# Kernel tuning notes

Measured on AMD Instinct MI355X. Metric: run time of the kernel, lower is better.

Reference implementation:

```python
import jax, jax.numpy as jnp
import numpy as np

N_HEADS = 8
MAX_PARTS = 8
TOKENS_PER_PART = 64
NUM_BLOCKS = 6
D_MODEL = 256
LN_EPS = 1e-5


def layernorm(x, w, b):
    mu = jnp.mean(x, axis=-1, keepdims=True)
    var = jnp.var(x, axis=-1, keepdims=True)
    return (x - mu) * jax.lax.rsqrt(var + LN_EPS) * w + b


def mha(q, k, v, in_w, in_b, out_w, out_b):
    # torch nn.MultiheadAttention: packed in_proj [3D, D], out_proj [D, D]
    D = q.shape[-1]
    dh = D // N_HEADS
    wq, wk, wv = in_w[:D], in_w[D:2 * D], in_w[2 * D:]
    bq, bk, bv = in_b[:D], in_b[D:2 * D], in_b[2 * D:]
    qp = q @ wq.T + bq  # [B, Sq, D]
    kp = k @ wk.T + bk
    vp = v @ wv.T + bv
    B, Sq, _ = qp.shape
    Sk = kp.shape[1]
    qh = qp.reshape(B, Sq, N_HEADS, dh).transpose(0, 2, 1, 3)
    kh = kp.reshape(B, Sk, N_HEADS, dh).transpose(0, 2, 1, 3)
    vh = vp.reshape(B, Sk, N_HEADS, dh).transpose(0, 2, 1, 3)
    scores = jnp.einsum('bhqd,bhkd->bhqk', qh, kh) / jnp.sqrt(jnp.asarray(dh, qp.dtype))
    attn = jax.nn.softmax(scores, axis=-1)
    out = jnp.einsum('bhqk,bhkd->bhqd', attn, vh)
    out = out.transpose(0, 2, 1, 3).reshape(B, Sq, D)
    return out @ out_w.T + out_b


def setup_inputs() -> dict:
    key = jax.random.key(0)
    ks = jax.random.split(key, 16)
    s = 0.02
    return {
        'feat': jax.random.normal(ks[0], (64, 49, 512), jnp.float32),
        'img_proj_w': jax.random.normal(ks[1], (256, 512), jnp.float32) * s,
        'img_proj_b': jnp.zeros((256,), jnp.float32),
        'init_part_tokens': jax.random.normal(ks[2], (512, 256), jnp.float32),
        'part_id_emb': jax.random.normal(ks[3], (8, 256), jnp.float32),
        'local_in_w': jax.random.normal(ks[4], (768, 256), jnp.float32) * s,
        'local_in_b': jnp.zeros((768,), jnp.float32),
        'local_out_w': jax.random.normal(ks[5], (256, 256), jnp.float32) * s,
        'local_out_b': jnp.zeros((256,), jnp.float32),
        'cross_in_w': jax.random.normal(ks[6], (768, 256), jnp.float32) * s,
        'cross_in_b': jnp.zeros((768,), jnp.float32),
        'cross_out_w': jax.random.normal(ks[7], (256, 256), jnp.float32) * s,
        'cross_out_b': jnp.zeros((256,), jnp.float32),
        'norm1_w': jnp.ones((6, 256), jnp.float32),
        'norm1_b': jnp.zeros((6, 256), jnp.float32),
        'norm2_w': jnp.ones((6, 256), jnp.float32),
        'norm2_b': jnp.zeros((6, 256), jnp.float32),
        'coord_w': jax.random.normal(ks[8], (3, 256), jnp.float32) * s,
        'coord_b': jnp.zeros((3,), jnp.float32),
    }


def reference(feat, img_proj_w, img_proj_b, init_part_tokens, part_id_emb,
              local_in_w, local_in_b, local_out_w, local_out_b,
              cross_in_w, cross_in_b, cross_out_w, cross_out_b,
              norm1_w, norm1_b, norm2_w, norm2_b, coord_w, coord_b):
    B = feat.shape[0]
    P, T, D = MAX_PARTS, TOKENS_PER_PART, D_MODEL
    img_tokens = feat @ img_proj_w.T + img_proj_b  # [B, 49, D]
    # broadcast part-id embedding over tokens_per_part
    pid = jnp.repeat(part_id_emb, T, axis=0)  # [P*T, D]
    st = jnp.broadcast_to(init_part_tokens + pid, (B, P * T, D))
    for i in range(NUM_BLOCKS):
        # block-diagonal local attention: fold parts into batch dim
        parts = st.reshape(B * P, T, D)
        local = mha(parts, parts, parts, local_in_w, local_in_b, local_out_w, local_out_b)
        local = local.reshape(B, P * T, D)
        st = layernorm(st + local, norm1_w[i], norm1_b[i])
        cross = mha(st, img_tokens, img_tokens, cross_in_w, cross_in_b, cross_out_w, cross_out_b)
        st = layernorm(st + cross, norm2_w[i], norm2_b[i])
    coords = st @ coord_w.T + coord_b
    return coords.reshape(B, P, T, 3)
```

## Files before the change

kernel.cpp:

```cpp
#include <hip/hip_runtime.h>
#include <hip/hip_bf16.h>


#define B_     64
#define P_     8
#define T_     64
#define S_     512
#define D_     256
#define H_     8
#define DH_    32
#define NIMG_  49
#define M_ST   32768
#define M_IMG  3136

#define AS1 __attribute__((address_space(1)))
#define AS3 __attribute__((address_space(3)))

typedef short bf16x8 __attribute__((ext_vector_type(8)));
typedef float f32x4  __attribute__((ext_vector_type(4)));

__device__ inline uint f2b_pk(float x, float y) {
    uint bx = __float_as_uint(x), by = __float_as_uint(y);
    bx = (bx + 0x7FFFu + ((bx >> 16) & 1u)) >> 16;
    by = (by + 0x7FFFu + ((by >> 16) & 1u)) >> 16;
    return bx | (by << 16);
}
__device__ inline ushort f2b(float x) {
    uint b = __float_as_uint(x);
    return (ushort)((b + 0x7FFFu + ((b >> 16) & 1u)) >> 16);
}
__device__ inline float b2f(ushort u) {
    return __uint_as_float(((uint)u) << 16);
}

__global__ __launch_bounds__(256) void cvt_bf16x4(
    const float4* __restrict__ in, uint2* __restrict__ out, int n4)
{
    int i = blockIdx.x * 256 + threadIdx.x;
    if (i < n4) {
        float4 v = in[i];
        out[i] = make_uint2(f2b_pk(v.x, v.y), f2b_pk(v.z, v.w));
    }
}

__global__ __launch_bounds__(256) void gemm_bf16(
    const ushort* __restrict__ A,
    const ushort* __restrict__ W,
    const float*  __restrict__ bias,
    ushort*       __restrict__ C,
    int M, int N, int K)
{
    __shared__ ushort smem[128 * 128];
    ushort* Asm = smem;
    ushort* Bsm = smem + 4096;

    const int tid  = threadIdx.x;
    const int lane = tid & 63;
    const int wave = tid >> 6;
    const int wr = wave >> 1, wc = wave & 1;
    const int row0 = blockIdx.x * 128, col0 = blockIdx.y * 128;

    f32x4 acc[4][4] = {};

    const int skc = (tid & 3) * 8;
    const int sr0 = tid >> 2;
    const int fr  = lane & 15;
    const int g   = lane >> 4;

    for (int k0 = 0; k0 < K; k0 += 32) {
        #pragma unroll
        for (int i = 0; i < 2; ++i) {
            const int r = sr0 + i * 64;
            const int e = (tid + i * 256) * 8;
            int ra = row0 + r; if (ra >= M) ra = M - 1;
            __builtin_amdgcn_global_load_lds(
                (const AS1 void*)(A + (size_t)ra * K + k0 + skc),
                (AS3 void*)&Asm[e], 16, 0, 0);
            __builtin_amdgcn_global_load_lds(
                (const AS1 void*)(W + (size_t)(col0 + r) * K + k0 + skc),
                (AS3 void*)&Bsm[e], 16, 0, 0);
        }
        __syncthreads();

        bf16x8 af[4], bf[4];
        #pragma unroll
        for (int i = 0; i < 4; ++i)
            af[i] = *reinterpret_cast<const bf16x8*>(&Asm[(wr * 64 + i * 16 + fr) * 32 + g * 8]);
        #pragma unroll
        for (int j = 0; j < 4; ++j)
            bf[j] = *reinterpret_cast<const bf16x8*>(&Bsm[(wc * 64 + j * 16 + fr) * 32 + g * 8]);
        #pragma unroll
        for (int i = 0; i < 4; ++i)
            #pragma unroll
            for (int j = 0; j < 4; ++j)
                acc[i][j] = __builtin_amdgcn_mfma_f32_16x16x32_bf16(
                    af[i], bf[j], acc[i][j], 0, 0, 0);
        __syncthreads();
    }

    float bn[4];
    #pragma unroll
    for (int j = 0; j < 4; ++j) bn[j] = bias[col0 + wc * 64 + j * 16 + fr];

    #pragma unroll
    for (int i = 0; i < 4; ++i)
        #pragma unroll
        for (int j = 0; j < 4; ++j)
            #pragma unroll
            for (int r = 0; r < 4; ++r)
                smem[(wr * 64 + i * 16 + g * 4 + r) * 128 + wc * 64 + j * 16 + fr] =
                    f2b(acc[i][j][r] + bn[j]);
    __syncthreads();

    #pragma unroll
    for (int it = 0; it < 8; ++it) {
        const int elem = (it * 256 + tid) * 8;
        const int lrow = elem >> 7, lcol = elem & 127;
        const int m = row0 + lrow;
        if (m < M)
            *reinterpret_cast<uint4*>(&C[(size_t)m * N + col0 + lcol]) =
                *reinterpret_cast<const uint4*>(&smem[elem]);
    }
}

__global__ __launch_bounds__(512, 4) void gemm_bf16_big(
    const ushort* __restrict__ A,
    const ushort* __restrict__ W,
    const float*  __restrict__ bias,
    ushort*       __restrict__ C,
    int N, int K)
{
    __shared__ ushort smem[16384];
    ushort* Asm = smem;
    ushort* Bsm = smem + 8192;

    const int tid  = threadIdx.x;
    const int lane = tid & 63;
    const int wave = tid >> 6;
    const int wr = wave >> 1, wc = wave & 1;
    const int row0 = blockIdx.x * 256, col0 = blockIdx.y * 128;

    f32x4 acc[4][4] = {};
    const int skc = (tid & 3) * 8;
    const int sr0 = tid >> 2;
    const int fr  = lane & 15;
    const int g   = lane >> 4;

    for (int k0 = 0; k0 < K; k0 += 32) {
        #pragma unroll
        for (int i = 0; i < 2; ++i) {
            const int r = sr0 + i * 128;
            __builtin_amdgcn_global_load_lds(
                (const AS1 void*)(A + (size_t)(row0 + r) * K + k0 + skc),
                (AS3 void*)&Asm[(tid + i * 512) * 8], 16, 0, 0);
        }
        __builtin_amdgcn_global_load_lds(
            (const AS1 void*)(W + (size_t)(col0 + sr0) * K + k0 + skc),
            (AS3 void*)&Bsm[tid * 8], 16, 0, 0);
        __syncthreads();

        bf16x8 af[4], bf[4];
        #pragma unroll
        for (int i = 0; i < 4; ++i)
            af[i] = *reinterpret_cast<const bf16x8*>(&Asm[(wr * 64 + i * 16 + fr) * 32 + g * 8]);
        #pragma unroll
        for (int j = 0; j < 4; ++j)
            bf[j] = *reinterpret_cast<const bf16x8*>(&Bsm[(wc * 64 + j * 16 + fr) * 32 + g * 8]);
        #pragma unroll
        for (int i = 0; i < 4; ++i)
            #pragma unroll
            for (int j = 0; j < 4; ++j)
                acc[i][j] = __builtin_amdgcn_mfma_f32_16x16x32_bf16(
                    af[i], bf[j], acc[i][j], 0, 0, 0);
        __syncthreads();
    }

    float bn[4];
    #pragma unroll
    for (int j = 0; j < 4; ++j) bn[j] = bias[col0 + wc * 64 + j * 16 + fr];

    #pragma unroll
    for (int h2 = 0; h2 < 2; ++h2) {
        if ((wr >> 1) == h2) {
            const int lwr = wr & 1;
            #pragma unroll
            for (int i = 0; i < 4; ++i)
                #pragma unroll
                for (int j = 0; j < 4; ++j)
                    #pragma unroll
                    for (int r = 0; r < 4; ++r)
                        smem[(lwr * 64 + i * 16 + g * 4 + r) * 128 + wc * 64 + j * 16 + fr] =
                            f2b(acc[i][j][r] + bn[j]);
        }
        __syncthreads();
        #pragma unroll
        for (int it = 0; it < 4; ++it) {
            const int elem = (it * 512 + tid) * 8;
            const int lrow = elem >> 7, lcol = elem & 127;
            *reinterpret_cast<uint4*>(
                &C[(size_t)(row0 + h2 * 128 + lrow) * N + col0 + lcol]) =
                *reinterpret_cast<const uint4*>(&smem[elem]);
        }
        __syncthreads();
    }
}

__global__ __launch_bounds__(256) void gemm_ln(
    const ushort* __restrict__ A,
    const ushort* __restrict__ W,
    const float*  __restrict__ bias,
    ushort*       __restrict__ stb,
    const float*  __restrict__ lnw,
    const float*  __restrict__ lnb)
{
    __shared__ ushort As[64 * 32];
    __shared__ ushort Bs[256 * 32];
    __shared__ ushort Cs[64 * 256];
    __shared__ float  redS[64][4];
    __shared__ float  redS2[64][4];

    const int tid  = threadIdx.x;
    const int lane = tid & 63;
    const int wc   = tid >> 6;
    const int fr = lane & 15, g = lane >> 4;
    const int row0 = blockIdx.x * 64;

    f32x4 acc[4][4] = {};
    const int skc = (tid & 3) * 8;
    const int sr  = tid >> 2;

    for (int k0 = 0; k0 < 256; k0 += 32) {
        __builtin_amdgcn_global_load_lds(
            (const AS1 void*)(A + (size_t)(row0 + sr) * 256 + k0 + skc),
            (AS3 void*)&As[tid * 8], 16, 0, 0);
        #pragma unroll
        for (int q = 0; q < 4; ++q)
            __builtin_amdgcn_global_load_lds(
                (const AS1 void*)(W + (size_t)(sr + q * 64) * 256 + k0 + skc),
                (AS3 void*)&Bs[(tid + q * 256) * 8], 16, 0, 0);
        __syncthreads();

        bf16x8 af[4], bf[4];
        #pragma unroll
        for (int i = 0; i < 4; ++i)
            af[i] = *reinterpret_cast<const bf16x8*>(&As[(i * 16 + fr) * 32 + g * 8]);
        #pragma unroll
        for (int j = 0; j < 4; ++j)
            bf[j] = *reinterpret_cast<const bf16x8*>(&Bs[(wc * 64 + j * 16 + fr) * 32 + g * 8]);
        #pragma unroll
        for (int i = 0; i < 4; ++i)
            #pragma unroll
            for (int j = 0; j < 4; ++j)
                acc[i][j] = __builtin_amdgcn_mfma_f32_16x16x32_bf16(
                    af[i], bf[j], acc[i][j], 0, 0, 0);
        __syncthreads();
    }

    int   col[4]; float bv[4], wv[4], lb[4];
    #pragma unroll
    for (int j = 0; j < 4; ++j) {
        col[j] = wc * 64 + j * 16 + fr;
        bv[j]  = bias[col[j]];
        wv[j]  = lnw[col[j]];
        lb[j]  = lnb[col[j]];
    }

    #pragma unroll
    for (int i = 0; i < 4; ++i)
        #pragma unroll
        for (int r = 0; r < 4; ++r) {
            const int rl = i * 16 + g * 4 + r;
            const size_t rb = (size_t)(row0 + rl) * 256;
            float s = 0.f, s2 = 0.f;
            #pragma unroll
            for (int j = 0; j < 4; ++j) {
                float x = acc[i][j][r] + bv[j] + b2f(stb[rb + col[j]]);
                acc[i][j][r] = x;
                s += x; s2 += x * x;
            }
            #pragma unroll
            for (int o = 1; o < 16; o <<= 1) {
                s  += __shfl_xor(s, o);
                s2 += __shfl_xor(s2, o);
            }
            if (fr == 0) { redS[rl][wc] = s; redS2[rl][wc] = s2; }
        }
    __syncthreads();

    #pragma unroll
    for (int i = 0; i < 4; ++i)
        #pragma unroll
        for (int r = 0; r < 4; ++r) {
            const int rl = i * 16 + g * 4 + r;
            const float ts  = redS[rl][0] + redS[rl][1] + redS[rl][2] + redS[rl][3];
            const float ts2 = redS2[rl][0] + redS2[rl][1] + redS2[rl][2] + redS2[rl][3];
            const float mean = ts * (1.f / 256.f);
            const float var  = ts2 * (1.f / 256.f) - mean * mean;
            const float rs   = rsqrtf(var + 1e-5f);
            #pragma unroll
            for (int j = 0; j < 4; ++j) {
                const float y = (acc[i][j][r] - mean) * rs * wv[j] + lb[j];
                Cs[rl * 256 + col[j]] = f2b(y);
            }
        }
    __syncthreads();

    #pragma unroll
    for (int it = 0; it < 8; ++it) {
        const int elem = (it * 256 + tid) * 8;
        const int rl = elem >> 8, c = elem & 255;
        *reinterpret_cast<uint4*>(&stb[(size_t)(row0 + rl) * 256 + c]) =
            *reinterpret_cast<const uint4*>(&Cs[elem]);
    }
}

template<int CROSS>
__global__ __launch_bounds__(256) void attn_mfma(
    const ushort* __restrict__ qsrc,
    const ushort* __restrict__ ksrc,
    const ushort* __restrict__ vsrc,
    ushort* __restrict__ out)
{
    constexpr int QSTR = CROSS ? 256 : 768;
    constexpr int KSTR = CROSS ? 256 : 768;

    const int bid = blockIdx.x;
    int qrow0, krow0;
    if (CROSS) { qrow0 = (bid >> 3) * 512 + (bid & 7) * 64; krow0 = (bid >> 3) * 49; }
    else       { qrow0 = bid * 64; krow0 = bid * 64; }

    __shared__ ushort P_lds[4][64][72];
    __shared__ ushort Vt_lds[4][32][72];
    ushort* Os = &P_lds[0][0][0];

    const int tid = threadIdx.x;
    const int w = tid >> 6, l = tid & 63;
    const int fr = l & 15, g = l >> 4;
    ushort (*P)[72]  = P_lds[w];
    ushort (*Vt)[72] = Vt_lds[w];

    f32x4 o2[2][4][2] = {};

    #pragma unroll
    for (int hh = 0; hh < 2; ++hh) {
        const int h = w + hh * 4;
        const int hoff = h * 32;

        bf16x8 kf[4], qf[4];
        #pragma unroll
        for (int i = 0; i < 4; ++i) {
            int t = 16 * i + fr;
            if (CROSS && t > 48) t = 48;
            kf[i] = *reinterpret_cast<const bf16x8*>(
                ksrc + (size_t)(krow0 + t) * KSTR + hoff + g * 8);
        }
        #pragma unroll
        for (int j = 0; j < 4; ++j)
            qf[j] = *reinterpret_cast<const bf16x8*>(
                qsrc + (size_t)(qrow0 + 16 * j + fr) * QSTR + hoff + g * 8);

        #pragma unroll
        for (int t2 = 0; t2 < 2; ++t2) {
            const int task = t2 * 64 + l;
            const int rp = task >> 2, cg = task & 3;
            int r0 = 2 * rp, r1 = r0 + 1;
            if (CROSS) { if (r0 > 48) r0 = 48; if (r1 > 48) r1 = 48; }
            const uint4 a = *reinterpret_cast<const uint4*>(
                vsrc + (size_t)(krow0 + r0) * KSTR + hoff + cg * 8);
            const uint4 b = *reinterpret_cast<const uint4*>(
                vsrc + (size_t)(krow0 + r1) * KSTR + hoff + cg * 8);
            const uint ac[4] = {a.x, a.y, a.z, a.w};
            const uint bc[4] = {b.x, b.y, b.z, b.w};
            #pragma unroll
            for (int k = 0; k < 4; ++k) {
                uint lo = (ac[k] & 0xFFFFu) | (bc[k] << 16);
                uint hi = (ac[k] >> 16)     | (bc[k] & 0xFFFF0000u);
                *reinterpret_cast<uint*>(&Vt[cg * 8 + 2 * k][2 * rp])     = lo;
                *reinterpret_cast<uint*>(&Vt[cg * 8 + 2 * k + 1][2 * rp]) = hi;
            }
        }

        f32x4 st_[4][4];
        #pragma unroll
        for (int i = 0; i < 4; ++i)
            #pragma unroll
            for (int j = 0; j < 4; ++j) {
                f32x4 z = {};
                st_[i][j] = __builtin_amdgcn_mfma_f32_16x16x32_bf16(
                    kf[i], qf[j], z, 0, 0, 0);
                st_[i][j] *= 0.17677669529663689f;
            }
        if (CROSS) {
            #pragma unroll
            for (int j = 0; j < 4; ++j)
                #pragma unroll
                for (int r = 0; r < 4; ++r)
                    if (r > 0 || g > 0) st_[3][j][r] = -1e30f;
        }

        #pragma unroll
        for (int j = 0; j < 4; ++j) {
            float mx = -1e30f;
            #pragma unroll
            for (int i = 0; i < 4; ++i)
                #pragma unroll
                for (int r = 0; r < 4; ++r) mx = fmaxf(mx, st_[i][j][r]);
            mx = fmaxf(mx, __shfl_xor(mx, 16));
            mx = fmaxf(mx, __shfl_xor(mx, 32));
            float sm = 0.f;
            #pragma unroll
            for (int i = 0; i < 4; ++i)
                #pragma unroll
                for (int r = 0; r < 4; ++r) {
                    float p = __expf(st_[i][j][r] - mx);
                    st_[i][j][r] = p;
                    sm += p;
                }
            sm += __shfl_xor(sm, 16);
            sm += __shfl_xor(sm, 32);
            const float inv = 1.f / sm;
            const int q = 16 * j + fr;
            #pragma unroll
            for (int i = 0; i < 4; ++i) {
                uint lo = f2b_pk(st_[i][j][0] * inv, st_[i][j][1] * inv);
                uint hi = f2b_pk(st_[i][j][2] * inv, st_[i][j][3] * inv);
                *reinterpret_cast<uint2*>(&P[q][16 * i + 4 * g]) = make_uint2(lo, hi);
            }
        }

        __syncthreads();

        #pragma unroll
        for (int s = 0; s < 2; ++s) {
            bf16x8 pa[4], vb[2];
            #pragma unroll
            for (int i = 0; i < 4; ++i)
                pa[i] = *reinterpret_cast<const bf16x8*>(&P[16 * i + fr][32 * s + 8 * g]);
            #pragma unroll
            for (int j2 = 0; j2 < 2; ++j2)
                vb[j2] = *reinterpret_cast<const bf16x8*>(&Vt[16 * j2 + fr][32 * s + 8 * g]);
            #pragma unroll
            for (int i = 0; i < 4; ++i)
                #pragma unroll
                for (int j2 = 0; j2 < 2; ++j2)
                    o2[hh][i][j2] = __builtin_amdgcn_mfma_f32_16x16x32_bf16(
                        pa[i], vb[j2], o2[hh][i][j2], 0, 0, 0);
        }
    }

    __syncthreads();

    #pragma unroll
    for (int hh = 0; hh < 2; ++hh)
        #pragma unroll
        for (int i = 0; i < 4; ++i)
            #pragma unroll
            for (int j2 = 0; j2 < 2; ++j2)
                #pragma unroll
                for (int r = 0; r < 4; ++r)
                    Os[(16 * i + 4 * g + r) * 256 + hh * 128 + w * 32 + 16 * j2 + fr] =
                        f2b(o2[hh][i][j2][r]);
    __syncthreads();

    #pragma unroll
    for (int it = 0; it < 8; ++it) {
        const int elem = (it * 256 + tid) * 8;
        const int lrow = elem >> 8, lcol = elem & 255;
        *reinterpret_cast<uint4*>(&out[(size_t)(qrow0 + lrow) * 256 + lcol]) =
            *reinterpret_cast<const uint4*>(&Os[elem]);
    }
}

__global__ __launch_bounds__(256) void init_st(
    ushort* __restrict__ stb,
    const float* __restrict__ init_tokens, const float* __restrict__ pid_emb)
{
    int i = blockIdx.x * 256 + threadIdx.x;
    int c = i & 63;
    int s = (i >> 6) & 511;
    int p = s >> 6;
    float4 v = *reinterpret_cast<const float4*>(&init_tokens[s * 256 + c * 4]);
    float4 e = *reinterpret_cast<const float4*>(&pid_emb[p * 256 + c * 4]);
    v.x += e.x; v.y += e.y; v.z += e.z; v.w += e.w;
    *reinterpret_cast<uint2*>(&stb[(size_t)i * 4]) =
        make_uint2(f2b_pk(v.x, v.y), f2b_pk(v.z, v.w));
}

__global__ __launch_bounds__(256) void coord_head(
    const ushort* __restrict__ stb, const float* __restrict__ w,
    const float* __restrict__ b, float* __restrict__ out)
{
    const int row = blockIdx.x * 8 + (threadIdx.x >> 5);
    const int l   = threadIdx.x & 31;
    const ushort* x = stb + (size_t)row * 256 + l * 8;
    uint4 xv = *reinterpret_cast<const uint4*>(x);
    float xf[8];
    const uint xc[4] = {xv.x, xv.y, xv.z, xv.w};
    #pragma unroll
    for (int k = 0; k < 4; ++k) {
        xf[2*k]   = __uint_as_float(xc[k] << 16);
        xf[2*k+1] = __uint_as_float(xc[k] & 0xFFFF0000u);
    }
    float acc[3];
    #pragma unroll
    for (int n = 0; n < 3; ++n) {
        const float* wn = w + n * 256 + l * 8;
        float4 w0 = *reinterpret_cast<const float4*>(wn);
        float4 w1 = *reinterpret_cast<const float4*>(wn + 4);
        acc[n] = xf[0]*w0.x + xf[1]*w0.y + xf[2]*w0.z + xf[3]*w0.w
               + xf[4]*w1.x + xf[5]*w1.y + xf[6]*w1.z + xf[7]*w1.w;
    }
    #pragma unroll
    for (int o = 16; o; o >>= 1)
        #pragma unroll
        for (int n = 0; n < 3; ++n) acc[n] += __shfl_xor(acc[n], o);
    if (l == 0) {
        #pragma unroll
        for (int n = 0; n < 3; ++n) out[(size_t)row * 3 + n] = acc[n] + b[n];
    }
}

extern "C" void kernel_launch(void* const* d_in, const int* in_sizes, int n_in,
                              void* d_out, int out_size, void* d_ws, size_t ws_size,
                              hipStream_t stream)
{
    const float* feat             = (const float*)d_in[0];
    const float* img_proj_w      = (const float*)d_in[1];
    const float* img_proj_b      = (const float*)d_in[2];
    const float* init_part_tokens = (const float*)d_in[3];
    const float* part_id_emb     = (const float*)d_in[4];
    const float* local_in_w      = (const float*)d_in[5];
    const float* local_in_b      = (const float*)d_in[6];
    const float* local_out_w     = (const float*)d_in[7];
    const float* local_out_b     = (const float*)d_in[8];
    const float* cross_in_w      = (const float*)d_in[9];
    const float* cross_in_b      = (const float*)d_in[10];
    const float* cross_out_w     = (const float*)d_in[11];
    const float* cross_out_b     = (const float*)d_in[12];
    const float* norm1_w         = (const float*)d_in[13];
    const float* norm1_b         = (const float*)d_in[14];
    const float* norm2_w         = (const float*)d_in[15];
    const float* norm2_b         = (const float*)d_in[16];
    const float* coord_w         = (const float*)d_in[17];
    const float* coord_b         = (const float*)d_in[18];
    float* out = (float*)d_out;

    ushort* stb  = (ushort*)d_ws;
    ushort* big  = stb  + (size_t)M_ST * D_;
    ushort* attn = big  + (size_t)M_ST * 3 * D_;
    ushort* fbf  = attn + (size_t)M_ST * D_;
    ushort* img  = fbf  + (size_t)M_IMG * 512;
    ushort* kimg = img  + (size_t)M_IMG * D_;
    ushort* vimg = kimg + (size_t)M_IMG * D_;
    ushort* lw_in  = vimg  + (size_t)M_IMG * D_;
    ushort* lw_out = lw_in  + 768 * 256;
    ushort* cw_in  = lw_out + 256 * 256;
    ushort* cw_out = cw_in  + 768 * 256;
    ushort* iw     = cw_out + 256 * 256;

    cvt_bf16x4<<<768*256/4/256, 256, 0, stream>>>((const float4*)local_in_w,  (uint2*)lw_in,  768*256/4);
    cvt_bf16x4<<<256*256/4/256, 256, 0, stream>>>((const float4*)local_out_w, (uint2*)lw_out, 256*256/4);
    cvt_bf16x4<<<768*256/4/256, 256, 0, stream>>>((const float4*)cross_in_w,  (uint2*)cw_in,  768*256/4);
    cvt_bf16x4<<<256*256/4/256, 256, 0, stream>>>((const float4*)cross_out_w, (uint2*)cw_out, 256*256/4);
    cvt_bf16x4<<<256*512/4/256, 256, 0, stream>>>((const float4*)img_proj_w,  (uint2*)iw,     256*512/4);
    cvt_bf16x4<<<(M_IMG*512/4 + 255)/256, 256, 0, stream>>>((const float4*)feat, (uint2*)fbf, M_IMG*512/4);

    gemm_bf16<<<dim3((M_IMG+127)/128, 2), 256, 0, stream>>>(fbf, iw, img_proj_b, img, M_IMG, 256, 512);
    gemm_bf16<<<dim3((M_IMG+127)/128, 2), 256, 0, stream>>>(img, cw_in + 256*256, cross_in_b + 256, kimg, M_IMG, 256, 256);
    gemm_bf16<<<dim3((M_IMG+127)/128, 2), 256, 0, stream>>>(img, cw_in + 512*256, cross_in_b + 512, vimg, M_IMG, 256, 256);
    init_st<<<M_ST * D_ / 4 / 256, 256, 0, stream>>>(stb, init_part_tokens, part_id_emb);

    for (int i = 0; i < 6; ++i) {
        gemm_bf16_big<<<dim3(M_ST/256, 6), 512, 0, stream>>>(stb, lw_in, local_in_b, big, 768, 256);
        attn_mfma<0><<<512, 256, 0, stream>>>(big, big + 256, big + 512, attn);
        gemm_ln<<<M_ST/64, 256, 0, stream>>>(attn, lw_out, local_out_b, stb,
                                             norm1_w + i*256, norm1_b + i*256);
        gemm_bf16_big<<<dim3(M_ST/256, 2), 512, 0, stream>>>(stb, cw_in, cross_in_b, big, 256, 256);
        attn_mfma<1><<<512, 256, 0, stream>>>(big, kimg, vimg, attn);
        gemm_ln<<<M_ST/64, 256, 0, stream>>>(attn, cw_out, cross_out_b, stb,
                                             norm2_w + i*256, norm2_b + i*256);
    }

    coord_head<<<M_ST / 8, 256, 0, stream>>>(stb, coord_w, coord_b, out);
}
```

Before: 725.1 us.

## Fuse attention with output projection and residual layernorm; merge image K/V GEMMs

The attention kernel now keeps its per-block attention output in shared memory (padded stride) and runs the out-projection GEMM, bias, residual add and layernorm in the same kernel, writing the result straight into the state buffer. This removes the intermediate attention buffer's global round trip and one kernel launch per sub-block. The image K and V projections are merged into a single GEMM producing an interleaved [M,512] buffer. The trade-off is higher register and LDS pressure in the fused kernel, which may lower occupancy, and only 512 blocks of 64 rows do the projection work.

```diff
diff --git a/kernel.cpp b/kernel.cpp
--- a/kernel.cpp
+++ b/kernel.cpp
@@ -12,6 +12,7 @@
 #define NIMG_  49
 #define M_ST   32768
 #define M_IMG  3136
+#define OSTR   264
 
 #define AS1 __attribute__((address_space(1)))
 #define AS3 __attribute__((address_space(3)))
@@ -205,124 +206,19 @@
     }
 }
 
-__global__ __launch_bounds__(256) void gemm_ln(
-    const ushort* __restrict__ A,
+template<int CROSS>
+__global__ __launch_bounds__(256) void attn_oln(
+    const ushort* __restrict__ qsrc,
+    const ushort* __restrict__ ksrc,
+    const ushort* __restrict__ vsrc,
     const ushort* __restrict__ W,
     const float*  __restrict__ bias,
     ushort*       __restrict__ stb,
     const float*  __restrict__ lnw,
     const float*  __restrict__ lnb)
 {
-    __shared__ ushort As[64 * 32];
-    __shared__ ushort Bs[256 * 32];
-    __shared__ ushort Cs[64 * 256];
-    __shared__ float  redS[64][4];
-    __shared__ float  redS2[64][4];
-
-    const int tid  = threadIdx.x;
-    const int lane = tid & 63;
-    const int wc   = tid >> 6;
-    const int fr = lane & 15, g = lane >> 4;
-    const int row0 = blockIdx.x * 64;
-
-    f32x4 acc[4][4] = {};
-    const int skc = (tid & 3) * 8;
-    const int sr  = tid >> 2;
-
-    for (int k0 = 0; k0 < 256; k0 += 32) {
-        __builtin_amdgcn_global_load_lds(
-            (const AS1 void*)(A + (size_t)(row0 + sr) * 256 + k0 + skc),
-            (AS3 void*)&As[tid * 8], 16, 0, 0);
-        #pragma unroll
-        for (int q = 0; q < 4; ++q)
-            __builtin_amdgcn_global_load_lds(
-                (const AS1 void*)(W + (size_t)(sr + q * 64) * 256 + k0 + skc),
-                (AS3 void*)&Bs[(tid + q * 256) * 8], 16, 0, 0);
-        __syncthreads();
-
-        bf16x8 af[4], bf[4];
-        #pragma unroll
-        for (int i = 0; i < 4; ++i)
-            af[i] = *reinterpret_cast<const bf16x8*>(&As[(i * 16 + fr) * 32 + g * 8]);
-        #pragma unroll
-        for (int j = 0; j < 4; ++j)
-            bf[j] = *reinterpret_cast<const bf16x8*>(&Bs[(wc * 64 + j * 16 + fr) * 32 + g * 8]);
-        #pragma unroll
-        for (int i = 0; i < 4; ++i)
-            #pragma unroll
-            for (int j = 0; j < 4; ++j)
-                acc[i][j] = __builtin_amdgcn_mfma_f32_16x16x32_bf16(
-                    af[i], bf[j], acc[i][j], 0, 0, 0);
-        __syncthreads();
-    }
-
-    int   col[4]; float bv[4], wv[4], lb[4];
-    #pragma unroll
-    for (int j = 0; j < 4; ++j) {
-        col[j] = wc * 64 + j * 16 + fr;
-        bv[j]  = bias[col[j]];
-        wv[j]  = lnw[col[j]];
-        lb[j]  = lnb[col[j]];
-    }
-
-    #pragma unroll
-    for (int i = 0; i < 4; ++i)
-        #pragma unroll
-        for (int r = 0; r < 4; ++r) {
-            const int rl = i * 16 + g * 4 + r;
-            const size_t rb = (size_t)(row0 + rl) * 256;
-            float s = 0.f, s2 = 0.f;
-            #pragma unroll
-            for (int j = 0; j < 4; ++j) {
-                float x = acc[i][j][r] + bv[j] + b2f(stb[rb + col[j]]);
-                acc[i][j][r] = x;
-                s += x; s2 += x * x;
-            }
-            #pragma unroll
-            for (int o = 1; o < 16; o <<= 1) {
-                s  += __shfl_xor(s, o);
-                s2 += __shfl_xor(s2, o);
-            }
-            if (fr == 0) { redS[rl][wc] = s; redS2[rl][wc] = s2; }
-        }
-    __syncthreads();
-
-    #pragma unroll
-    for (int i = 0; i < 4; ++i)
-        #pragma unroll
-        for (int r = 0; r < 4; ++r) {
-            const int rl = i * 16 + g * 4 + r;
-            const float ts  = redS[rl][0] + redS[rl][1] + redS[rl][2] + redS[rl][3];
-            const float ts2 = redS2[rl][0] + redS2[rl][1] + redS2[rl][2] + redS2[rl][3];
-            const float mean = ts * (1.f / 256.f);
-            const float var  = ts2 * (1.f / 256.f) - mean * mean;
-            const float rs   = rsqrtf(var + 1e-5f);
-            #pragma unroll
-            for (int j = 0; j < 4; ++j) {
-                const float y = (acc[i][j][r] - mean) * rs * wv[j] + lb[j];
-                Cs[rl * 256 + col[j]] = f2b(y);
-            }
-        }
-    __syncthreads();
-
-    #pragma unroll
-    for (int it = 0; it < 8; ++it) {
-        const int elem = (it * 256 + tid) * 8;
-        const int rl = elem >> 8, c = elem & 255;
-        *reinterpret_cast<uint4*>(&stb[(size_t)(row0 + rl) * 256 + c]) =
-            *reinterpret_cast<const uint4*>(&Cs[elem]);
-    }
-}
-
-template<int CROSS>
-__global__ __launch_bounds__(256) void attn_mfma(
-    const ushort* __restrict__ qsrc,
-    const ushort* __restrict__ ksrc,
-    const ushort* __restrict__ vsrc,
-    ushort* __restrict__ out)
-{
     constexpr int QSTR = CROSS ? 256 : 768;
-    constexpr int KSTR = CROSS ? 256 : 768;
+    constexpr int KSTR = CROSS ? 512 : 768;
 
     const int bid = blockIdx.x;
     int qrow0, krow0;
@@ -331,7 +227,10 @@
 
     __shared__ ushort P_lds[4][64][72];
     __shared__ ushort Vt_lds[4][32][72];
+    __shared__ float  redS[64][4];
+    __shared__ float  redS2[64][4];
     ushort* Os = &P_lds[0][0][0];
+    ushort* Bs = &Vt_lds[0][0][0];
 
     const int tid = threadIdx.x;
     const int w = tid >> 6, l = tid & 63;
@@ -458,16 +357,94 @@
             for (int j2 = 0; j2 < 2; ++j2)
                 #pragma unroll
                 for (int r = 0; r < 4; ++r)
-                    Os[(16 * i + 4 * g + r) * 256 + hh * 128 + w * 32 + 16 * j2 + fr] =
+                    Os[(16 * i + 4 * g + r) * OSTR + hh * 128 + w * 32 + 16 * j2 + fr] =
                         f2b(o2[hh][i][j2][r]);
+
+    const int skc = (tid & 3) * 8;
+    const int srB = tid >> 2;
+
+    f32x4 acc[4][4] = {};
+    for (int k0 = 0; k0 < 256; k0 += 32) {
+        #pragma unroll
+        for (int q = 0; q < 4; ++q)
+            __builtin_amdgcn_global_load_lds(
+                (const AS1 void*)(W + (size_t)(srB + q * 64) * 256 + k0 + skc),
+                (AS3 void*)&Bs[(tid + q * 256) * 8], 16, 0, 0);
+        __syncthreads();
+
+        bf16x8 af[4], bf[4];
+        #pragma unroll
+        for (int i = 0; i < 4; ++i)
+            af[i] = *reinterpret_cast<const bf16x8*>(&Os[(i * 16 + fr) * OSTR + k0 + g * 8]);
+        #pragma unroll
+        for (int j = 0; j < 4; ++j)
+            bf[j] = *reinterpret_cast<const bf16x8*>(&Bs[(w * 64 + j * 16 + fr) * 32 + g * 8]);
+        #pragma unroll
+        for (int i = 0; i < 4; ++i)
+            #pragma unroll
+            for (int j = 0; j < 4; ++j)
+                acc[i][j] = __builtin_amdgcn_mfma_f32_16x16x32_bf16(
+                    af[i], bf[j], acc[i][j], 0, 0, 0);
+        __syncthreads();
+    }
+
+    int   col[4]; float bv[4], wv[4], lb[4];
+    #pragma unroll
+    for (int j = 0; j < 4; ++j) {
+        col[j] = w * 64 + j * 16 + fr;
+        bv[j]  = bias[col[j]];
+        wv[j]  = lnw[col[j]];
+        lb[j]  = lnb[col[j]];
+    }
+
+    const int row0 = qrow0;
+
+    #pragma unroll
+    for (int i = 0; i < 4; ++i)
+        #pragma unroll
+        for (int r = 0; r < 4; ++r) {
+            const int rl = i * 16 + g * 4 + r;
+            const size_t rb = (size_t)(row0 + rl) * 256;
+            float s = 0.f, s2 = 0.f;
+            #pragma unroll
+            for (int j = 0; j < 4; ++j) {
+                float x = acc[i][j][r] + bv[j] + b2f(stb[rb + col[j]]);
+                acc[i][j][r] = x;
+                s += x; s2 += x * x;
+            }
+            #pragma unroll
+            for (int o = 1; o < 16; o <<= 1) {
+                s  += __shfl_xor(s, o);
+                s2 += __shfl_xor(s2, o);
+            }
+            if (fr == 0) { redS[rl][w] = s; redS2[rl][w] = s2; }
+        }
     __syncthreads();
 
     #pragma unroll
+    for (int i = 0; i < 4; ++i)
+        #pragma unroll
+        for (int r = 0; r < 4; ++r) {
+            const int rl = i * 16 + g * 4 + r;
+            const float ts  = redS[rl][0] + redS[rl][1] + redS[rl][2] + redS[rl][3];
+            const float ts2 = redS2[rl][0] + redS2[rl][1] + redS2[rl][2] + redS2[rl][3];
+            const float mean = ts * (1.f / 256.f);
+            const float var  = ts2 * (1.f / 256.f) - mean * mean;
+            const float rs   = rsqrtf(var + 1e-5f);
+            #pragma unroll
+            for (int j = 0; j < 4; ++j) {
+                const float y = (acc[i][j][r] - mean) * rs * wv[j] + lb[j];
+                Os[rl * OSTR + col[j]] = f2b(y);
+            }
+        }
+    __syncthreads();
+
+    #pragma unroll
     for (int it = 0; it < 8; ++it) {
-        const int elem = (it * 256 + tid) * 8;
-        const int lrow = elem >> 8, lcol = elem & 255;
-        *reinterpret_cast<uint4*>(&out[(size_t)(qrow0 + lrow) * 256 + lcol]) =
-            *reinterpret_cast<const uint4*>(&Os[elem]);
+        const int e = it * 256 + tid;
+        const int lrow = e >> 5, lcol = (e & 31) * 8;
+        *reinterpret_cast<uint4*>(&stb[(size_t)(row0 + lrow) * 256 + lcol]) =
+            *reinterpret_cast<const uint4*>(&Os[lrow * OSTR + lcol]);
     }
 }
 
@@ -547,12 +524,10 @@
 
     ushort* stb  = (ushort*)d_ws;
     ushort* big  = stb  + (size_t)M_ST * D_;
-    ushort* attn = big  + (size_t)M_ST * 3 * D_;
-    ushort* fbf  = attn + (size_t)M_ST * D_;
+    ushort* kv   = big  + (size_t)M_ST * 3 * D_;
+    ushort* fbf  = kv   + (size_t)M_IMG * 512;
     ushort* img  = fbf  + (size_t)M_IMG * 512;
-    ushort* kimg = img  + (size_t)M_IMG * D_;
-    ushort* vimg = kimg + (size_t)M_IMG * D_;
-    ushort* lw_in  = vimg  + (size_t)M_IMG * D_;
+    ushort* lw_in  = img   + (size_t)M_IMG * D_;
     ushort* lw_out = lw_in  + 768 * 256;
     ushort* cw_in  = lw_out + 256 * 256;
     ushort* cw_out = cw_in  + 768 * 256;
@@ -566,18 +541,18 @@
     cvt_bf16x4<<<(M_IMG*512/4 + 255)/256, 256, 0, stream>>>((const float4*)feat, (uint2*)fbf, M_IMG*512/4);
 
     gemm_bf16<<<dim3((M_IMG+127)/128, 2), 256, 0, stream>>>(fbf, iw, img_proj_b, img, M_IMG, 256, 512);
-    gemm_bf16<<<dim3((M_IMG+127)/128, 2), 256, 0, stream>>>(img, cw_in + 256*256, cross_in_b + 256, kimg, M_IMG, 256, 256);
-    gemm_bf16<<<dim3((M_IMG+127)/128, 2), 256, 0, stream>>>(img, cw_in + 512*256, cross_in_b + 512, vimg, M_IMG, 256, 256);
+    gemm_bf16<<<dim3((M_IMG+127)/128, 4), 256, 0, stream>>>(
+        img, cw_in + 256*256, cross_in_b + 256, kv, M_IMG, 512, 256);
     init_st<<<M_ST * D_ / 4 / 256, 256, 0, stream>>>(stb, init_part_tokens, part_id_emb);
 
     for (int i = 0; i < 6; ++i) {
         gemm_bf16_big<<<dim3(M_ST/256, 6), 512, 0, stream>>>(stb, lw_in, local_in_b, big, 768, 256);
-        attn_mfma<0><<<512, 256, 0, stream>>>(big, big + 256, big + 512, attn);
-        gemm_ln<<<M_ST/64, 256, 0, stream>>>(attn, lw_out, local_out_b, stb,
+        attn_oln<0><<<512, 256, 0, stream>>>(big, big + 256, big + 512,
+                                             lw_out, local_out_b, stb,
                                              norm1_w + i*256, norm1_b + i*256);
         gemm_bf16_big<<<dim3(M_ST/256, 2), 512, 0, stream>>>(stb, cw_in, cross_in_b, big, 256, 256);
-        attn_mfma<1><<<512, 256, 0, stream>>>(big, kimg, vimg, attn);
-        gemm_ln<<<M_ST/64, 256, 0, stream>>>(attn, cw_out, cross_out_b, stb,
+        attn_oln<1><<<512, 256, 0, stream>>>(big, kv, kv + 256,
+                                             cw_out, cross_out_b, stb,
                                              norm2_w + i*256, norm2_b + i*256);
     }
 
```

New measurement: 659.8 us. 1.1x faster.
